# Kernel tuning notes

Measured on AMD Instinct MI355X. Metric: run time of the kernel, lower is better.

The kernel has to match this reference:

```python
import jax, jax.numpy as jnp
import numpy as np

B, CIN, H, W = 4, 2048, 65, 65
NC, INNER, QL = 19, 256, 2975
TEMP = 0.2
EPS = 1e-5


def _conv(x, w, dil=1, pad=0):
    return jax.lax.conv_general_dilated(
        x, w, (1, 1), [(pad, pad), (pad, pad)], rhs_dilation=(dil, dil),
        dimension_numbers=('NCHW', 'OIHW', 'NCHW'))


def _bn_relu(x, g, b):
    # training-mode BatchNorm2d (batch statistics over N,H,W) + ReLU
    m = x.mean(axis=(0, 2, 3), keepdims=True)
    v = x.var(axis=(0, 2, 3), keepdims=True)
    return jax.nn.relu(g[None, :, None, None] * (x - m) * jax.lax.rsqrt(v + EPS)
                       + b[None, :, None, None])


def setup_inputs() -> dict:
    key = jax.random.key(0)
    ks = jax.random.split(key, 12)
    rn = lambda k, s, sc=0.02: jax.random.normal(k, s, jnp.float32) * sc
    inp = {
        'x': jax.random.normal(ks[0], (B, CIN, H, W), jnp.float32),
        # ASPP: global-pool branch (1x1), 1x1 branch, three dilated 3x3 branches
        'w_gp': rn(ks[1], (INNER, CIN, 1, 1)), 'g_gp': jnp.ones(INNER), 'b_gp': jnp.zeros(INNER),
        'w_1x1': rn(ks[2], (INNER, CIN, 1, 1)), 'g_1x1': jnp.ones(INNER), 'b_1x1': jnp.zeros(INNER),
        'w_d12': rn(ks[3], (INNER, CIN, 3, 3)), 'g_d12': jnp.ones(INNER), 'b_d12': jnp.zeros(INNER),
        'w_d24': rn(ks[4], (INNER, CIN, 3, 3)), 'g_d24': jnp.ones(INNER), 'b_d24': jnp.zeros(INNER),
        'w_d36': rn(ks[5], (INNER, CIN, 3, 3)), 'g_d36': jnp.ones(INNER), 'b_d36': jnp.zeros(INNER),
        # head: 3x3 conv on 5*INNER concat -> 256, BN, ReLU (Dropout2d = identity)
        'w_head': rn(ks[6], (256, 5 * INNER, 3, 3)), 'g_head': jnp.ones(256), 'b_head': jnp.zeros(256),
        # final 1x1 classifier
        'w_fin': rn(ks[7], (NC, 256, 1, 1)), 'b_fin': jnp.zeros(NC),
    }
    q = jax.random.normal(ks[8], (NC, INNER, QL), jnp.float32)
    inp['queues'] = q / jnp.linalg.norm(q, axis=1, keepdims=True)  # normalize dim=0 per-class
    return inp


def reference(x, w_gp, g_gp, b_gp, w_1x1, g_1x1, b_1x1,
              w_d12, g_d12, b_d12, w_d24, g_d24, b_d24, w_d36, g_d36, b_d36,
              w_head, g_head, b_head, w_fin, b_fin, queues):
    bsz = x.shape[0]
    # ---- ASPP ----
    gp = x.mean(axis=(2, 3), keepdims=True)                       # global avg pool
    br0 = _bn_relu(_conv(gp, w_gp), g_gp, b_gp)
    br0 = jnp.broadcast_to(br0, (bsz, INNER, x.shape[2], x.shape[3]))
    br1 = _bn_relu(_conv(x, w_1x1), g_1x1, b_1x1)
    br2 = _bn_relu(_conv(x, w_d12, 12, 12), g_d12, b_d12)
    br3 = _bn_relu(_conv(x, w_d24, 24, 24), g_d24, b_d24)
    br4 = _bn_relu(_conv(x, w_d36, 36, 36), g_d36, b_d36)
    aspp_out = jnp.concatenate([br0, br1, br2, br3, br4], axis=1)  # (B, 5*INNER, H, W)
    # ---- head + final (Dropout2d(0.1) treated as identity) ----
    fea = _bn_relu(_conv(aspp_out, w_head, 1, 1), g_head, b_head)  # (B, 256, H, W)
    res = _conv(fea, w_fin) + b_fin[None, :, None, None]           # (B, NC, H, W)
    # ---- construct_region: per-class masked mean over ALL batch pixels ----
    pred = jnp.argmax(res, axis=1).reshape(bsz, -1)                # (B, HW)
    onehot = (pred[:, None, :] == jnp.arange(NC)[None, :, None]).astype(fea.dtype)  # (B,NC,HW)
    feaf = fea.reshape(bsz, 256, -1)                               # (B, 256, HW)
    sums = jnp.einsum('bcp,bkp->kc', feaf, onehot)                 # (NC, 256)
    counts = onehot.sum(axis=(0, 2))                               # (NC,)
    keys = sums / jnp.maximum(counts, 1.0)[:, None]
    keys = keys / jnp.maximum(jnp.linalg.norm(keys, axis=1, keepdims=True), 1e-12)
    present = counts > 0
    # ---- contrast loss: (query . queue)/INNER == mean over channels ----
    sims = jnp.einsum('kc,jcl->kjl', keys, jax.lax.stop_gradient(queues)) / INNER  # (NC,NC,QL)
    a = sims / TEMP
    lse_rows = jax.nn.logsumexp(a, axis=2)                         # (NC, NC)
    neg_rows = jnp.where(jnp.eye(NC, dtype=bool), -jnp.inf, lse_rows)
    lse_neg = jax.nn.logsumexp(neg_rows, axis=1)                   # (NC,) lse over 18*QL negatives
    pos = a[jnp.arange(NC), jnp.arange(NC)]                        # (NC, QL) diagonal class sims
    # CE with label 0 over [pos_i, negs] == logaddexp(pos_i, lse_neg) - pos_i, averaged over QL
    loss_per = (jnp.logaddexp(pos, lse_neg[:, None]) - pos).mean(axis=1)
    contrast_loss = jnp.sum(jnp.where(present, loss_per, 0.0))
    return res, contrast_loss
```

## Files before the change

### kernel.cpp

```cpp
#include <hip/hip_runtime.h>
#include <stdint.h>

#define HW_   4225
#define NPIX_ 16900
#define NC_   19
#define QL_   2975
#define EPSF  1e-5f

#define AS1 __attribute__((address_space(1)))
#define AS3 __attribute__((address_space(3)))

typedef __bf16 bf16x8 __attribute__((ext_vector_type(8)));
typedef float  f32x4  __attribute__((ext_vector_type(4)));

__device__ __forceinline__ unsigned short f2bf(float f) {
    union { float f; unsigned u; } v; v.f = f;
    unsigned u = v.u;
    return (unsigned short)((u + 0x7fffu + ((u >> 16) & 1u)) >> 16);
}
__device__ __forceinline__ float bf2f(unsigned short b) {
    union { unsigned u; float f; } v; v.u = ((unsigned)b) << 16;
    return v.f;
}

__global__ void k_transpose_x(const float* __restrict__ x, unsigned short* __restrict__ xt,
                              float* __restrict__ gp_acc) {
    __shared__ float T[64][66];
    __shared__ float red[256];
    int b  = blockIdx.z;
    int c0 = blockIdx.y * 64;
    int p0 = blockIdx.x * 64;
    int tx = threadIdx.x & 63, ty = threadIdx.x >> 6;
    bool pv = (p0 + tx) < HW_;
    #pragma unroll
    for (int i = 0; i < 16; ++i) {
        int cl = i * 4 + ty;
        T[cl][tx] = pv ? x[((size_t)(b * 2048 + c0 + cl)) * HW_ + p0 + tx] : 0.f;
    }
    __syncthreads();
    #pragma unroll
    for (int i = 0; i < 16; ++i) {
        int pl = i * 4 + ty;
        int p = p0 + pl;
        if (p < HW_) xt[((size_t)(b * HW_ + p)) * 2048 + c0 + tx] = f2bf(T[tx][pl]);
    }
    float s = 0.f;
    #pragma unroll
    for (int k = 0; k < 16; ++k) s += T[tx][ty * 16 + k];
    red[threadIdx.x] = s;
    __syncthreads();
    if (threadIdx.x < 64) {
        float t = red[threadIdx.x] + red[64 + threadIdx.x] + red[128 + threadIdx.x] + red[192 + threadIdx.x];
        atomicAdd(&gp_acc[b * 2048 + c0 + threadIdx.x], t);
    }
}

__global__ void k_wreorder(const float* __restrict__ src, unsigned short* __restrict__ dst,
                           int ci_n, int ntaps) {
    int ci  = blockIdx.x * 256 + threadIdx.x;
    int co  = blockIdx.y, tap = blockIdx.z;
    dst[((size_t)tap * 256 + co) * ci_n + ci] =
        f2bf(src[((size_t)co * ci_n + ci) * ntaps + tap]);
}

__global__ __launch_bounds__(256) void k_conv_gemm(
    const unsigned short* __restrict__ xin, const unsigned short* __restrict__ wr_base,
    unsigned short* __restrict__ out, const unsigned short* __restrict__ zp,
    int cin, int ostride, int is_head)
{
    __shared__ unsigned short As[128 * 64];
    __shared__ unsigned short Bs[128 * 64];
    __shared__ int tapvalid;
    const int tid = threadIdx.x;
    const int bz = blockIdx.z;
    int dil, ntaps, coff;
    if (is_head) { dil = 1; ntaps = 9; coff = 0; }
    else         { dil = 12 * bz; ntaps = bz ? 9 : 1; coff = 256 * (bz + 1); }
    const int mbase = blockIdx.x * 128;
    const int nbase = blockIdx.y * 128;

    const int wv = tid >> 6, lane = tid & 63;
    const int wm = wv >> 1, wn = wv & 1;
    const int quad = lane >> 4, lrow = lane & 15;
    const int sw = lrow & 7;

    const int rowoff = lane >> 3;
    const int lchunk = (lane & 7) ^ rowoff;

    int py4[4], px4[4], pb4[4], pix4[4];
    #pragma unroll
    for (int q = 0; q < 4; ++q) {
        int r = 32 * wv + 8 * q + rowoff;
        int pix = mbase + r;
        pix4[q] = pix;
        int pb = pix / HW_;
        int pr = pix - pb * HW_;
        py4[q] = pr / 65; px4[q] = pr - py4[q] * 65; pb4[q] = pb;
    }

    f32x4 acc[4][4];
    #pragma unroll
    for (int i = 0; i < 4; ++i)
        #pragma unroll
        for (int j = 0; j < 4; ++j) acc[i][j] = (f32x4){0.f, 0.f, 0.f, 0.f};

    for (int tap = 0; tap < ntaps; ++tap) {
        int dy = (ntaps == 1) ? 0 : (tap / 3 - 1) * dil;
        int dx = (ntaps == 1) ? 0 : (tap % 3 - 1) * dil;

        const unsigned short* aptr[4];
        const unsigned short* bptr[4];
        bool av[4];
        bool anyv = false;
        #pragma unroll
        for (int q = 0; q < 4; ++q) {
            int ys = py4[q] + dy, xs = px4[q] + dx;
            bool v = (pix4[q] < NPIX_) && ((unsigned)ys < 65u) && ((unsigned)xs < 65u);
            av[q] = v; anyv |= v;
            aptr[q] = v ? (xin + ((size_t)(pb4[q] * HW_ + ys * 65 + xs)) * cin + lchunk * 8) : zp;
            bptr[q] = wr_base + ((size_t)((bz * 9 + tap) * 256 + nbase + 32 * wv + 8 * q + rowoff)) * cin + lchunk * 8;
        }

        if (tid == 0) tapvalid = 0;
        __syncthreads();
        if (anyv) tapvalid = 1;
        __syncthreads();
        if (!tapvalid) continue;

        for (int kc = 0; kc < cin; kc += 64) {
            __syncthreads();
            #pragma unroll
            for (int q = 0; q < 4; ++q) {
                const unsigned short* pa = av[q] ? (aptr[q] + kc) : zp;
                __builtin_amdgcn_global_load_lds(
                    (const AS1 void*)pa,
                    (AS3 void*)(As + (32 * wv + 8 * q) * 64), 16, 0, 0);
                __builtin_amdgcn_global_load_lds(
                    (const AS1 void*)(bptr[q] + kc),
                    (AS3 void*)(Bs + (32 * wv + 8 * q) * 64), 16, 0, 0);
            }
            __syncthreads();

            #pragma unroll
            for (int kk = 0; kk < 2; ++kk) {
                const int koch = kk * 4 + quad;
                bf16x8 af[4], bfv[4];
                #pragma unroll
                for (int i = 0; i < 4; ++i) {
                    int row = wm * 64 + i * 16 + lrow;
                    af[i] = *(const bf16x8*)(As + row * 64 + ((koch ^ sw) << 3));
                }
                #pragma unroll
                for (int j = 0; j < 4; ++j) {
                    int row = wn * 64 + j * 16 + lrow;
                    bfv[j] = *(const bf16x8*)(Bs + row * 64 + ((koch ^ sw) << 3));
                }
                #pragma unroll
                for (int i = 0; i < 4; ++i)
                    #pragma unroll
                    for (int j = 0; j < 4; ++j)
                        acc[i][j] = __builtin_amdgcn_mfma_f32_16x16x32_bf16(
                            af[i], bfv[j], acc[i][j], 0, 0, 0);
            }
        }
    }

    #pragma unroll
    for (int i = 0; i < 4; ++i) {
        int prow = mbase + wm * 64 + i * 16 + quad * 4;
        #pragma unroll
        for (int r = 0; r < 4; ++r) {
            int p = prow + r;
            if (p < NPIX_) {
                unsigned short* orow = out + (size_t)p * ostride + coff + nbase + wn * 64 + lrow;
                #pragma unroll
                for (int j = 0; j < 4; ++j) orow[j * 16] = f2bf(acc[i][j][r]);
            }
        }
    }
}

__global__ void k_stats(const unsigned short* __restrict__ buf, int stride, int coff,
                        float* __restrict__ sums, float* __restrict__ sumsq) {
    int c = blockIdx.y * 256 + threadIdx.x;
    int p0 = blockIdx.x * 130, p1 = p0 + 130;
    float s = 0.f, q = 0.f;
    for (int p = p0; p < p1; ++p) {
        float v = bf2f(buf[(size_t)p * stride + coff + c]);
        s += v; q += v * v;
    }
    atomicAdd(&sums[c], s);
    atomicAdd(&sumsq[c], q);
}

__global__ void k_br0mv(const float* __restrict__ gp, const float* __restrict__ wgp,
                        float* __restrict__ pre) {
    __shared__ float red[256];
    int co = blockIdx.x, t = threadIdx.x;
    float s0 = 0, s1 = 0, s2 = 0, s3 = 0;
    for (int ci = t; ci < 2048; ci += 256) {
        float w = wgp[(size_t)co * 2048 + ci];
        s0 += w * gp[ci];        s1 += w * gp[2048 + ci];
        s2 += w * gp[4096 + ci]; s3 += w * gp[6144 + ci];
    }
    #pragma unroll
    for (int b = 0; b < 4; ++b) {
        float s = (b == 0) ? s0 : (b == 1) ? s1 : (b == 2) ? s2 : s3;
        red[t] = s; __syncthreads();
        for (int st = 128; st; st >>= 1) { if (t < st) red[t] += red[t + st]; __syncthreads(); }
        if (t == 0) pre[b * 256 + co] = red[0] * (1.0f / HW_);
        __syncthreads();
    }
}

__global__ void k_br0bn(const float* __restrict__ pre, const float* __restrict__ g,
                        const float* __restrict__ bb, float* __restrict__ post) {
    int t = threadIdx.x;
    float v0 = pre[t], v1 = pre[256 + t], v2 = pre[512 + t], v3 = pre[768 + t];
    float m = 0.25f * (v0 + v1 + v2 + v3);
    float var = 0.25f * (v0 * v0 + v1 * v1 + v2 * v2 + v3 * v3) - m * m;
    float sc = g[t] * rsqrtf(var + EPSF), sh = bb[t] - m * sc;
    post[t]       = fmaxf(v0 * sc + sh, 0.f);
    post[256 + t] = fmaxf(v1 * sc + sh, 0.f);
    post[512 + t] = fmaxf(v2 * sc + sh, 0.f);
    post[768 + t] = fmaxf(v3 * sc + sh, 0.f);
}

__global__ void k_norm_aspp(unsigned short* __restrict__ buf,
                            const float* __restrict__ sums, const float* __restrict__ sumsq,
                            const float* __restrict__ g1, const float* __restrict__ b1,
                            const float* __restrict__ g2, const float* __restrict__ b2,
                            const float* __restrict__ g3, const float* __restrict__ b3,
                            const float* __restrict__ g4, const float* __restrict__ b4,
                            const float* __restrict__ br0) {
    int cg = blockIdx.y, t = threadIdx.x;
    int p0 = blockIdx.x * 130, p1 = p0 + 130;
    if (cg == 0) {
        for (int p = p0; p < p1; ++p) {
            int b = p / HW_;
            buf[(size_t)p * 1280 + t] = f2bf(br0[b * 256 + t]);
        }
    } else {
        int c = (cg - 1) * 256 + t;
        float m = sums[c] * (1.f / NPIX_);
        float var = sumsq[c] * (1.f / NPIX_) - m * m;
        const float* g  = (cg == 1) ? g1 : (cg == 2) ? g2 : (cg == 3) ? g3 : g4;
        const float* bb = (cg == 1) ? b1 : (cg == 2) ? b2 : (cg == 3) ? b3 : b4;
        float sc = g[t] * rsqrtf(var + EPSF), sh = bb[t] - m * sc;
        for (int p = p0; p < p1; ++p) {
            size_t idx = (size_t)p * 1280 + cg * 256 + t;
            float v = bf2f(buf[idx]) * sc + sh;
            buf[idx] = f2bf(fmaxf(v, 0.f));
        }
    }
}

__global__ void k_norm_head(unsigned short* __restrict__ buf,
                            const float* __restrict__ sums, const float* __restrict__ sumsq,
                            const float* __restrict__ g, const float* __restrict__ bb) {
    int t = threadIdx.x;
    float m = sums[t] * (1.f / NPIX_);
    float var = sumsq[t] * (1.f / NPIX_) - m * m;
    float sc = g[t] * rsqrtf(var + EPSF), sh = bb[t] - m * sc;
    int p0 = blockIdx.x * 130, p1 = p0 + 130;
    for (int p = p0; p < p1; ++p) {
        size_t idx = (size_t)p * 256 + t;
        float v = bf2f(buf[idx]) * sc + sh;
        buf[idx] = f2bf(fmaxf(v, 0.f));
    }
}

__global__ void k_final(const unsigned short* __restrict__ fea, const float* __restrict__ wfin,
                        const float* __restrict__ bfin, float* __restrict__ outres) {
    int idx = blockIdx.x * 256 + threadIdx.x;
    if (idx >= NPIX_ * NC_) return;
    int p = idx / NC_, k = idx - p * NC_;
    const unsigned short* f = fea + (size_t)p * 256;
    const float* w = wfin + k * 256;
    float acc = 0.f;
    for (int c = 0; c < 256; c += 8) {
        uint4 q = *(const uint4*)(f + c);
        unsigned u0 = q.x, u1 = q.y, u2 = q.z, u3 = q.w;
        acc += bf2f((unsigned short)(u0 & 0xffff)) * w[c + 0];
        acc += bf2f((unsigned short)(u0 >> 16))    * w[c + 1];
        acc += bf2f((unsigned short)(u1 & 0xffff)) * w[c + 2];
        acc += bf2f((unsigned short)(u1 >> 16))    * w[c + 3];
        acc += bf2f((unsigned short)(u2 & 0xffff)) * w[c + 4];
        acc += bf2f((unsigned short)(u2 >> 16))    * w[c + 5];
        acc += bf2f((unsigned short)(u3 & 0xffff)) * w[c + 6];
        acc += bf2f((unsigned short)(u3 >> 16))    * w[c + 7];
    }
    acc += bfin[k];
    int b = p / HW_, yx = p - b * HW_;
    outres[(size_t)(b * NC_ + k) * HW_ + yx] = acc;
}

__global__ void k_argmax(const float* __restrict__ res, int* __restrict__ pred) {
    int p = blockIdx.x * 256 + threadIdx.x;
    if (p >= NPIX_) return;
    int b = p / HW_, yx = p - b * HW_;
    const float* r = res + (size_t)b * NC_ * HW_ + yx;
    float best = r[0]; int bi = 0;
    #pragma unroll
    for (int k = 1; k < NC_; ++k) {
        float v = r[(size_t)k * HW_];
        if (v > best) { best = v; bi = k; }
    }
    pred[p] = bi;
}

__global__ void k_keysums(const unsigned short* __restrict__ fea, const int* __restrict__ pred,
                          float* __restrict__ sums, float* __restrict__ counts) {
    __shared__ float acc[256 * NC_];
    __shared__ float cnt[NC_];
    int t = threadIdx.x;
    #pragma unroll
    for (int k = 0; k < NC_; ++k) acc[t * NC_ + k] = 0.f;
    if (t < NC_) cnt[t] = 0.f;
    __syncthreads();
    int p0 = blockIdx.x * 130, p1 = p0 + 130;
    for (int p = p0; p < p1; ++p) {
        int k = pred[p];
        float v = bf2f(fea[(size_t)p * 256 + t]);
        acc[t * NC_ + k] += v;
        if (t == 0) cnt[k] += 1.f;
    }
    __syncthreads();
    #pragma unroll
    for (int k = 0; k < NC_; ++k) atomicAdd(&sums[k * 256 + t], acc[t * NC_ + k]);
    if (t < NC_) atomicAdd(&counts[t], cnt[t]);
}

__global__ void k_keys(const float* __restrict__ sums, const float* __restrict__ counts,
                       float* __restrict__ keys) {
    __shared__ float red[256];
    int t = threadIdx.x;
    for (int k = 0; k < NC_; ++k) {
        float v = sums[k * 256 + t] / fmaxf(counts[k], 1.f);
        red[t] = v * v; __syncthreads();
        for (int s = 128; s; s >>= 1) { if (t < s) red[t] += red[t + s]; __syncthreads(); }
        float inv = 1.f / fmaxf(sqrtf(red[0]), 1e-12f);
        keys[k * 256 + t] = v * inv;
        __syncthreads();
    }
}

__global__ void k_sims(const float* __restrict__ keys, const float* __restrict__ queues,
                       float* __restrict__ Sexp, float* __restrict__ pos_a) {
    __shared__ float kl[NC_ * 256];
    __shared__ float red[256];
    int t = threadIdx.x;
    int j = blockIdx.x, lc = blockIdx.y;
    #pragma unroll
    for (int k = 0; k < NC_; ++k) kl[k * 256 + t] = keys[k * 256 + t];
    __syncthreads();
    int l = lc * 256 + t;
    bool lv = l < QL_;
    float a[NC_];
    #pragma unroll
    for (int k = 0; k < NC_; ++k) a[k] = 0.f;
    if (lv) {
        const float* q = queues + (size_t)j * 256 * QL_ + l;
        for (int c = 0; c < 256; ++c) {
            float qv = q[(size_t)c * QL_];
            #pragma unroll
            for (int k = 0; k < NC_; ++k) a[k] += kl[k * 256 + c] * qv;
        }
    }
    const float invt = 1.f / (256.f * 0.2f);
    if (lv) pos_a[j * QL_ + l] = a[j] * invt;
    for (int k = 0; k < NC_; ++k) {
        float e = lv ? __expf(a[k] * invt) : 0.f;
        red[t] = e; __syncthreads();
        for (int s = 128; s; s >>= 1) { if (t < s) red[t] += red[t + s]; __syncthreads(); }
        if (t == 0) atomicAdd(&Sexp[k * NC_ + j], red[0]);
        __syncthreads();
    }
}

__global__ void k_loss(const float* __restrict__ Sexp, const float* __restrict__ pos_a,
                       const float* __restrict__ counts, float* __restrict__ out_loss) {
    __shared__ float red[256];
    __shared__ float lseneg[NC_];
    int t = threadIdx.x;
    if (t < NC_) {
        float s = 0.f;
        for (int j = 0; j < NC_; ++j) if (j != t) s += Sexp[t * NC_ + j];
        lseneg[t] = logf(s);
    }
    __syncthreads();
    float total = 0.f;
    for (int k = 0; k < NC_; ++k) {
        float L = lseneg[k];
        float s = 0.f;
        for (int l = t; l < QL_; l += 256) {
            float pos = pos_a[k * QL_ + l];
            float m = fmaxf(pos, L);
            s += logf(__expf(pos - m) + __expf(L - m)) + m - pos;
        }
        red[t] = s; __syncthreads();
        for (int st = 128; st; st >>= 1) { if (t < st) red[t] += red[t + st]; __syncthreads(); }
        if (t == 0 && counts[k] > 0.f) total += red[0] * (1.f / QL_);
        __syncthreads();
    }
    if (t == 0) *out_loss = total;
}

extern "C" void kernel_launch(void* const* d_in, const int* in_sizes, int n_in,
                              void* d_out, int out_size, void* d_ws, size_t ws_size,
                              hipStream_t stream) {
    const float* x      = (const float*)d_in[0];
    const float* w_gp   = (const float*)d_in[1];
    const float* g_gp   = (const float*)d_in[2];
    const float* b_gp   = (const float*)d_in[3];
    const float* w_1x1  = (const float*)d_in[4];
    const float* g_1x1  = (const float*)d_in[5];
    const float* b_1x1  = (const float*)d_in[6];
    const float* w_d12  = (const float*)d_in[7];
    const float* g_d12  = (const float*)d_in[8];
    const float* b_d12  = (const float*)d_in[9];
    const float* w_d24  = (const float*)d_in[10];
    const float* g_d24  = (const float*)d_in[11];
    const float* b_d24  = (const float*)d_in[12];
    const float* w_d36  = (const float*)d_in[13];
    const float* g_d36  = (const float*)d_in[14];
    const float* b_d36  = (const float*)d_in[15];
    const float* w_head = (const float*)d_in[16];
    const float* g_head = (const float*)d_in[17];
    const float* b_head = (const float*)d_in[18];
    const float* w_fin  = (const float*)d_in[19];
    const float* b_fin  = (const float*)d_in[20];
    const float* queues = (const float*)d_in[21];

    char* ws = (char*)d_ws;
    size_t off = 0;
    auto alloc = [&](size_t bytes) { void* p = ws + off; off += (bytes + 255) & ~(size_t)255; return p; };

    unsigned short* x_t     = (unsigned short*)alloc((size_t)4 * HW_ * 2048 * 2);
    unsigned short* wr_aspp = (unsigned short*)alloc((size_t)4 * 9 * 256 * 2048 * 2);
    unsigned short* wr_head = (unsigned short*)alloc((size_t)9 * 256 * 1280 * 2);
    unsigned short* aspp    = (unsigned short*)alloc((size_t)NPIX_ * 1280 * 2);
    unsigned short* headb   = (unsigned short*)alloc((size_t)NPIX_ * 256 * 2);
    float* br0pre  = (float*)alloc(1024 * 4);
    float* br0post = (float*)alloc(1024 * 4);
    int*   pred    = (int*)alloc((size_t)NPIX_ * 4);
    float* pos_a   = (float*)alloc((size_t)NC_ * QL_ * 4);
    float* zbase       = (float*)alloc(16060 * 4);
    unsigned short* zp = (unsigned short*)zbase;
    float* gp          = zbase + 64;
    float* aspp_sums   = zbase + 8256;
    float* aspp_sumsq  = zbase + 9280;
    float* head_sums   = zbase + 10304;
    float* head_sumsq  = zbase + 10560;
    float* key_sums    = zbase + 10816;
    float* counts      = zbase + 15680;
    float* Sexp        = zbase + 15699;
    (void)ws_size; (void)in_sizes; (void)n_in; (void)out_size;

    float* res  = (float*)d_out;
    float* loss = (float*)d_out + (size_t)NPIX_ * NC_;

    hipMemsetAsync(zbase, 0, 16060 * 4, stream);

    k_transpose_x<<<dim3(67, 32, 4), 256, 0, stream>>>(x, x_t, gp);

    k_wreorder<<<dim3(8, 256, 1), 256, 0, stream>>>(w_1x1, wr_aspp, 2048, 1);
    k_wreorder<<<dim3(8, 256, 9), 256, 0, stream>>>(w_d12, wr_aspp + (size_t)1 * 9 * 256 * 2048, 2048, 9);
    k_wreorder<<<dim3(8, 256, 9), 256, 0, stream>>>(w_d24, wr_aspp + (size_t)2 * 9 * 256 * 2048, 2048, 9);
    k_wreorder<<<dim3(8, 256, 9), 256, 0, stream>>>(w_d36, wr_aspp + (size_t)3 * 9 * 256 * 2048, 2048, 9);
    k_wreorder<<<dim3(5, 256, 9), 256, 0, stream>>>(w_head, wr_head, 1280, 9);

    k_conv_gemm<<<dim3(133, 2, 4), 256, 0, stream>>>(x_t, wr_aspp, aspp, zp, 2048, 1280, 0);

    k_stats<<<dim3(130, 4), 256, 0, stream>>>(aspp, 1280, 256, aspp_sums, aspp_sumsq);
    k_br0mv<<<256, 256, 0, stream>>>(gp, w_gp, br0pre);
    k_br0bn<<<1, 256, 0, stream>>>(br0pre, g_gp, b_gp, br0post);
    k_norm_aspp<<<dim3(130, 5), 256, 0, stream>>>(aspp, aspp_sums, aspp_sumsq,
        g_1x1, b_1x1, g_d12, b_d12, g_d24, b_d24, g_d36, b_d36, br0post);

    k_conv_gemm<<<dim3(133, 2, 1), 256, 0, stream>>>(aspp, wr_head, headb, zp, 1280, 256, 1);
    k_stats<<<dim3(130, 1), 256, 0, stream>>>(headb, 256, 0, head_sums, head_sumsq);
    k_norm_head<<<130, 256, 0, stream>>>(headb, head_sums, head_sumsq, g_head, b_head);

    k_final<<<(NPIX_ * NC_ + 255) / 256, 256, 0, stream>>>(headb, w_fin, b_fin, res);
    k_argmax<<<(NPIX_ + 255) / 256, 256, 0, stream>>>(res, pred);
    k_keysums<<<130, 256, 0, stream>>>(headb, pred, key_sums, counts);
    k_keys<<<1, 256, 0, stream>>>(key_sums, counts, (float*)br0pre);
    k_sims<<<dim3(NC_, 12), 256, 0, stream>>>((float*)br0pre, queues, Sexp, pos_a);
    k_loss<<<1, 256, 0, stream>>>(Sexp, pos_a, counts, loss);
}
```

Before: 1.405 ms.

## Widen conv GEMM tile to full 256 outputs and split head taps with atomics

New measurement: 1.539 ms. 1.09x slower.

```diff
diff --git a/kernel.cpp b/kernel.cpp
--- a/kernel.cpp
+++ b/kernel.cpp
@@ -63,27 +63,30 @@
         f2bf(src[((size_t)co * ci_n + ci) * ntaps + tap]);
 }
 
-__global__ __launch_bounds__(256) void k_conv_gemm(
-    const unsigned short* __restrict__ xin, const unsigned short* __restrict__ wr_base,
-    unsigned short* __restrict__ out, const unsigned short* __restrict__ zp,
-    int cin, int ostride, int is_head)
+__global__ __launch_bounds__(256) void k_conv_os(
+    const unsigned short* __restrict__ xin, const unsigned short* __restrict__ wr,
+    unsigned short* __restrict__ outb, float* __restrict__ acc_out,
+    const unsigned short* __restrict__ zp, int cin, int is_head)
 {
     __shared__ unsigned short As[128 * 64];
-    __shared__ unsigned short Bs[128 * 64];
+    __shared__ unsigned short Bs[256 * 64];
     __shared__ int tapvalid;
     const int tid = threadIdx.x;
-    const int bz = blockIdx.z;
-    int dil, ntaps, coff;
-    if (is_head) { dil = 1; ntaps = 9; coff = 0; }
-    else         { dil = 12 * bz; ntaps = bz ? 9 : 1; coff = 256 * (bz + 1); }
+    int dil, tapbeg, tapend, coff, ostride;
+    const unsigned short* wrb;
+    if (is_head) {
+        dil = 1; tapbeg = blockIdx.y * 3; tapend = tapbeg + 3; coff = 0; ostride = 256;
+        wrb = wr;
+    } else {
+        int bz = 3 - blockIdx.y;
+        dil = 12 * bz; tapbeg = 0; tapend = bz ? 9 : 1; coff = 256 * (bz + 1); ostride = 1280;
+        wrb = wr + (size_t)bz * 9 * 256 * cin;
+    }
     const int mbase = blockIdx.x * 128;
-    const int nbase = blockIdx.y * 128;
-
     const int wv = tid >> 6, lane = tid & 63;
     const int wm = wv >> 1, wn = wv & 1;
     const int quad = lane >> 4, lrow = lane & 15;
     const int sw = lrow & 7;
-
     const int rowoff = lane >> 3;
     const int lchunk = (lane & 7) ^ rowoff;
 
@@ -98,18 +101,17 @@
         py4[q] = pr / 65; px4[q] = pr - py4[q] * 65; pb4[q] = pb;
     }
 
-    f32x4 acc[4][4];
+    f32x4 acc[4][8];
     #pragma unroll
     for (int i = 0; i < 4; ++i)
         #pragma unroll
-        for (int j = 0; j < 4; ++j) acc[i][j] = (f32x4){0.f, 0.f, 0.f, 0.f};
-
-    for (int tap = 0; tap < ntaps; ++tap) {
-        int dy = (ntaps == 1) ? 0 : (tap / 3 - 1) * dil;
-        int dx = (ntaps == 1) ? 0 : (tap % 3 - 1) * dil;
+        for (int j = 0; j < 8; ++j) acc[i][j] = (f32x4){0.f, 0.f, 0.f, 0.f};
+
+    for (int tap = tapbeg; tap < tapend; ++tap) {
+        int dy = (tap / 3 - 1) * dil;
+        int dx = (tap % 3 - 1) * dil;
 
         const unsigned short* aptr[4];
-        const unsigned short* bptr[4];
         bool av[4];
         bool anyv = false;
         #pragma unroll
@@ -118,14 +120,14 @@
             bool v = (pix4[q] < NPIX_) && ((unsigned)ys < 65u) && ((unsigned)xs < 65u);
             av[q] = v; anyv |= v;
             aptr[q] = v ? (xin + ((size_t)(pb4[q] * HW_ + ys * 65 + xs)) * cin + lchunk * 8) : zp;
-            bptr[q] = wr_base + ((size_t)((bz * 9 + tap) * 256 + nbase + 32 * wv + 8 * q + rowoff)) * cin + lchunk * 8;
-        }
-
+        }
         if (tid == 0) tapvalid = 0;
         __syncthreads();
         if (anyv) tapvalid = 1;
         __syncthreads();
         if (!tapvalid) continue;
+
+        const unsigned short* bbase = wrb + (size_t)tap * 256 * cin + lchunk * 8;
 
         for (int kc = 0; kc < cin; kc += 64) {
             __syncthreads();
@@ -135,30 +137,33 @@
                 __builtin_amdgcn_global_load_lds(
                     (const AS1 void*)pa,
                     (AS3 void*)(As + (32 * wv + 8 * q) * 64), 16, 0, 0);
+            }
+            #pragma unroll
+            for (int q = 0; q < 8; ++q) {
                 __builtin_amdgcn_global_load_lds(
-                    (const AS1 void*)(bptr[q] + kc),
-                    (AS3 void*)(Bs + (32 * wv + 8 * q) * 64), 16, 0, 0);
+                    (const AS1 void*)(bbase + (size_t)(64 * wv + 8 * q) * cin + kc),
+                    (AS3 void*)(Bs + (64 * wv + 8 * q) * 64), 16, 0, 0);
             }
             __syncthreads();
 
             #pragma unroll
             for (int kk = 0; kk < 2; ++kk) {
                 const int koch = kk * 4 + quad;
-                bf16x8 af[4], bfv[4];
+                bf16x8 af[4], bfv[8];
                 #pragma unroll
                 for (int i = 0; i < 4; ++i) {
                     int row = wm * 64 + i * 16 + lrow;
                     af[i] = *(const bf16x8*)(As + row * 64 + ((koch ^ sw) << 3));
                 }
                 #pragma unroll
-                for (int j = 0; j < 4; ++j) {
-                    int row = wn * 64 + j * 16 + lrow;
+                for (int j = 0; j < 8; ++j) {
+                    int row = wn * 128 + j * 16 + lrow;
                     bfv[j] = *(const bf16x8*)(Bs + row * 64 + ((koch ^ sw) << 3));
                 }
                 #pragma unroll
                 for (int i = 0; i < 4; ++i)
                     #pragma unroll
-                    for (int j = 0; j < 4; ++j)
+                    for (int j = 0; j < 8; ++j)
                         acc[i][j] = __builtin_amdgcn_mfma_f32_16x16x32_bf16(
                             af[i], bfv[j], acc[i][j], 0, 0, 0);
             }
@@ -172,9 +177,15 @@
         for (int r = 0; r < 4; ++r) {
             int p = prow + r;
             if (p < NPIX_) {
-                unsigned short* orow = out + (size_t)p * ostride + coff + nbase + wn * 64 + lrow;
-                #pragma unroll
-                for (int j = 0; j < 4; ++j) orow[j * 16] = f2bf(acc[i][j][r]);
+                if (is_head) {
+                    float* orow = acc_out + (size_t)p * 256 + wn * 128 + lrow;
+                    #pragma unroll
+                    for (int j = 0; j < 8; ++j) atomicAdd(&orow[j * 16], acc[i][j][r]);
+                } else {
+                    unsigned short* orow = outb + (size_t)p * ostride + coff + wn * 128 + lrow;
+                    #pragma unroll
+                    for (int j = 0; j < 8; ++j) orow[j * 16] = f2bf(acc[i][j][r]);
+                }
             }
         }
     }
@@ -187,6 +198,19 @@
     float s = 0.f, q = 0.f;
     for (int p = p0; p < p1; ++p) {
         float v = bf2f(buf[(size_t)p * stride + coff + c]);
+        s += v; q += v * v;
+    }
+    atomicAdd(&sums[c], s);
+    atomicAdd(&sumsq[c], q);
+}
+
+__global__ void k_stats_f32(const float* __restrict__ buf,
+                            float* __restrict__ sums, float* __restrict__ sumsq) {
+    int c = threadIdx.x;
+    int p0 = blockIdx.x * 130, p1 = p0 + 130;
+    float s = 0.f, q = 0.f;
+    for (int p = p0; p < p1; ++p) {
+        float v = buf[(size_t)p * 256 + c];
         s += v; q += v * v;
     }
     atomicAdd(&sums[c], s);
@@ -255,7 +279,7 @@
     }
 }
 
-__global__ void k_norm_head(unsigned short* __restrict__ buf,
+__global__ void k_norm_head(const float* __restrict__ accum, unsigned short* __restrict__ fea,
                             const float* __restrict__ sums, const float* __restrict__ sumsq,
                             const float* __restrict__ g, const float* __restrict__ bb) {
     int t = threadIdx.x;
@@ -265,8 +289,7 @@
     int p0 = blockIdx.x * 130, p1 = p0 + 130;
     for (int p = p0; p < p1; ++p) {
         size_t idx = (size_t)p * 256 + t;
-        float v = bf2f(buf[idx]) * sc + sh;
-        buf[idx] = f2bf(fmaxf(v, 0.f));
+        fea[idx] = f2bf(fmaxf(accum[idx] * sc + sh, 0.f));
     }
 }
 
@@ -455,6 +478,7 @@
     float* key_sums    = zbase + 10816;
     float* counts      = zbase + 15680;
     float* Sexp        = zbase + 15699;
+    float* head_acc = (float*)wr_aspp;
     (void)ws_size; (void)in_sizes; (void)n_in; (void)out_size;
 
     float* res  = (float*)d_out;
@@ -470,7 +494,7 @@
     k_wreorder<<<dim3(8, 256, 9), 256, 0, stream>>>(w_d36, wr_aspp + (size_t)3 * 9 * 256 * 2048, 2048, 9);
     k_wreorder<<<dim3(5, 256, 9), 256, 0, stream>>>(w_head, wr_head, 1280, 9);
 
-    k_conv_gemm<<<dim3(133, 2, 4), 256, 0, stream>>>(x_t, wr_aspp, aspp, zp, 2048, 1280, 0);
+    k_conv_os<<<dim3(133, 4), 256, 0, stream>>>(x_t, wr_aspp, aspp, nullptr, zp, 2048, 0);
 
     k_stats<<<dim3(130, 4), 256, 0, stream>>>(aspp, 1280, 256, aspp_sums, aspp_sumsq);
     k_br0mv<<<256, 256, 0, stream>>>(gp, w_gp, br0pre);
@@ -478,9 +502,10 @@
     k_norm_aspp<<<dim3(130, 5), 256, 0, stream>>>(aspp, aspp_sums, aspp_sumsq,
         g_1x1, b_1x1, g_d12, b_d12, g_d24, b_d24, g_d36, b_d36, br0post);
 
-    k_conv_gemm<<<dim3(133, 2, 1), 256, 0, stream>>>(aspp, wr_head, headb, zp, 1280, 256, 1);
-    k_stats<<<dim3(130, 1), 256, 0, stream>>>(headb, 256, 0, head_sums, head_sumsq);
-    k_norm_head<<<130, 256, 0, stream>>>(headb, head_sums, head_sumsq, g_head, b_head);
+    hipMemsetAsync(head_acc, 0, (size_t)NPIX_ * 256 * 4, stream);
+    k_conv_os<<<dim3(133, 3), 256, 0, stream>>>(aspp, wr_head, nullptr, head_acc, zp, 1280, 1);
+    k_stats_f32<<<130, 256, 0, stream>>>(head_acc, head_sums, head_sumsq);
+    k_norm_head<<<130, 256, 0, stream>>>(head_acc, headb, head_sums, head_sumsq, g_head, b_head);
 
     k_final<<<(NPIX_ * NC_ + 255) / 256, 256, 0, stream>>>(headb, w_fin, b_fin, res);
     k_argmax<<<(NPIX_ + 255) / 256, 256, 0, stream>>>(res, pred);
```

## Split head conv taps across grid z with fp32 partials; fuse final conv and argmax

Applied to the files above, without the earlier changes.

New measurement: 1.429 ms. No clear change (+1.7%).

```diff
diff --git a/kernel.cpp b/kernel.cpp
--- a/kernel.cpp
+++ b/kernel.cpp
@@ -64,18 +64,26 @@
 }
 
 __global__ __launch_bounds__(256) void k_conv_gemm(
-    const unsigned short* __restrict__ xin, const unsigned short* __restrict__ wr_base,
-    unsigned short* __restrict__ out, const unsigned short* __restrict__ zp,
-    int cin, int ostride, int is_head)
+    const unsigned short* __restrict__ xin, const unsigned short* __restrict__ wr,
+    unsigned short* __restrict__ outb, float* __restrict__ outf,
+    const unsigned short* __restrict__ zp, int cin, int ostride, int mode)
 {
     __shared__ unsigned short As[128 * 64];
     __shared__ unsigned short Bs[128 * 64];
     __shared__ int tapvalid;
     const int tid = threadIdx.x;
     const int bz = blockIdx.z;
-    int dil, ntaps, coff;
-    if (is_head) { dil = 1; ntaps = 9; coff = 0; }
-    else         { dil = 12 * bz; ntaps = bz ? 9 : 1; coff = 256 * (bz + 1); }
+    int dil, tapbeg, tapend, coff;
+    const unsigned short* wrb;
+    float* outfg = nullptr;
+    if (mode == 0) {
+        dil = 12 * bz; tapbeg = 0; tapend = bz ? 9 : 1; coff = 256 * (bz + 1);
+        wrb = wr + (size_t)bz * 9 * 256 * cin;
+    } else {
+        dil = 1; tapbeg = 3 * bz; tapend = tapbeg + 3; coff = 0;
+        wrb = wr;
+        outfg = outf + (size_t)bz * NPIX_ * 256;
+    }
     const int mbase = blockIdx.x * 128;
     const int nbase = blockIdx.y * 128;
 
@@ -83,7 +91,6 @@
     const int wm = wv >> 1, wn = wv & 1;
     const int quad = lane >> 4, lrow = lane & 15;
     const int sw = lrow & 7;
-
     const int rowoff = lane >> 3;
     const int lchunk = (lane & 7) ^ rowoff;
 
@@ -104,9 +111,9 @@
         #pragma unroll
         for (int j = 0; j < 4; ++j) acc[i][j] = (f32x4){0.f, 0.f, 0.f, 0.f};
 
-    for (int tap = 0; tap < ntaps; ++tap) {
-        int dy = (ntaps == 1) ? 0 : (tap / 3 - 1) * dil;
-        int dx = (ntaps == 1) ? 0 : (tap % 3 - 1) * dil;
+    for (int tap = tapbeg; tap < tapend; ++tap) {
+        int dy = (tap / 3 - 1) * dil;
+        int dx = (tap % 3 - 1) * dil;
 
         const unsigned short* aptr[4];
         const unsigned short* bptr[4];
@@ -118,7 +125,7 @@
             bool v = (pix4[q] < NPIX_) && ((unsigned)ys < 65u) && ((unsigned)xs < 65u);
             av[q] = v; anyv |= v;
             aptr[q] = v ? (xin + ((size_t)(pb4[q] * HW_ + ys * 65 + xs)) * cin + lchunk * 8) : zp;
-            bptr[q] = wr_base + ((size_t)((bz * 9 + tap) * 256 + nbase + 32 * wv + 8 * q + rowoff)) * cin + lchunk * 8;
+            bptr[q] = wrb + ((size_t)(tap * 256 + nbase + 32 * wv + 8 * q + rowoff)) * cin + lchunk * 8;
         }
 
         if (tid == 0) tapvalid = 0;
@@ -172,9 +179,15 @@
         for (int r = 0; r < 4; ++r) {
             int p = prow + r;
             if (p < NPIX_) {
-                unsigned short* orow = out + (size_t)p * ostride + coff + nbase + wn * 64 + lrow;
-                #pragma unroll
-                for (int j = 0; j < 4; ++j) orow[j * 16] = f2bf(acc[i][j][r]);
+                if (mode == 0) {
+                    unsigned short* orow = outb + (size_t)p * ostride + coff + nbase + wn * 64 + lrow;
+                    #pragma unroll
+                    for (int j = 0; j < 4; ++j) orow[j * 16] = f2bf(acc[i][j][r]);
+                } else {
+                    float* orow = outfg + (size_t)p * 256 + nbase + wn * 64 + lrow;
+                    #pragma unroll
+                    for (int j = 0; j < 4; ++j) orow[j * 16] = acc[i][j][r];
+                }
             }
         }
     }
@@ -187,6 +200,21 @@
     float s = 0.f, q = 0.f;
     for (int p = p0; p < p1; ++p) {
         float v = bf2f(buf[(size_t)p * stride + coff + c]);
+        s += v; q += v * v;
+    }
+    atomicAdd(&sums[c], s);
+    atomicAdd(&sumsq[c], q);
+}
+
+__global__ void k_stats_head(const float* __restrict__ part,
+                             float* __restrict__ sums, float* __restrict__ sumsq) {
+    const size_t NP = (size_t)NPIX_ * 256;
+    int c = threadIdx.x;
+    int p0 = blockIdx.x * 130, p1 = p0 + 130;
+    float s = 0.f, q = 0.f;
+    for (int p = p0; p < p1; ++p) {
+        size_t idx = (size_t)p * 256 + c;
+        float v = part[idx] + part[idx + NP] + part[idx + 2 * NP];
         s += v; q += v * v;
     }
     atomicAdd(&sums[c], s);
@@ -255,9 +283,10 @@
     }
 }
 
-__global__ void k_norm_head(unsigned short* __restrict__ buf,
+__global__ void k_norm_head(const float* __restrict__ part, unsigned short* __restrict__ fea,
                             const float* __restrict__ sums, const float* __restrict__ sumsq,
                             const float* __restrict__ g, const float* __restrict__ bb) {
+    const size_t NP = (size_t)NPIX_ * 256;
     int t = threadIdx.x;
     float m = sums[t] * (1.f / NPIX_);
     float var = sumsq[t] * (1.f / NPIX_) - m * m;
@@ -265,46 +294,40 @@
     int p0 = blockIdx.x * 130, p1 = p0 + 130;
     for (int p = p0; p < p1; ++p) {
         size_t idx = (size_t)p * 256 + t;
-        float v = bf2f(buf[idx]) * sc + sh;
-        buf[idx] = f2bf(fmaxf(v, 0.f));
-    }
-}
-
-__global__ void k_final(const unsigned short* __restrict__ fea, const float* __restrict__ wfin,
-                        const float* __restrict__ bfin, float* __restrict__ outres) {
-    int idx = blockIdx.x * 256 + threadIdx.x;
-    if (idx >= NPIX_ * NC_) return;
-    int p = idx / NC_, k = idx - p * NC_;
+        float v = part[idx] + part[idx + NP] + part[idx + 2 * NP];
+        fea[idx] = f2bf(fmaxf(v * sc + sh, 0.f));
+    }
+}
+
+__global__ __launch_bounds__(256) void k_final_argmax(
+    const unsigned short* __restrict__ fea, const float* __restrict__ wfin,
+    const float* __restrict__ bfin, float* __restrict__ outres, int* __restrict__ pred) {
+    int p = blockIdx.x * 256 + threadIdx.x;
+    if (p >= NPIX_) return;
     const unsigned short* f = fea + (size_t)p * 256;
-    const float* w = wfin + k * 256;
-    float acc = 0.f;
+    float acc[NC_];
+    #pragma unroll
+    for (int k = 0; k < NC_; ++k) acc[k] = bfin[k];
     for (int c = 0; c < 256; c += 8) {
         uint4 q = *(const uint4*)(f + c);
-        unsigned u0 = q.x, u1 = q.y, u2 = q.z, u3 = q.w;
-        acc += bf2f((unsigned short)(u0 & 0xffff)) * w[c + 0];
-        acc += bf2f((unsigned short)(u0 >> 16))    * w[c + 1];
-        acc += bf2f((unsigned short)(u1 & 0xffff)) * w[c + 2];
-        acc += bf2f((unsigned short)(u1 >> 16))    * w[c + 3];
-        acc += bf2f((unsigned short)(u2 & 0xffff)) * w[c + 4];
-        acc += bf2f((unsigned short)(u2 >> 16))    * w[c + 5];
-        acc += bf2f((unsigned short)(u3 & 0xffff)) * w[c + 6];
-        acc += bf2f((unsigned short)(u3 >> 16))    * w[c + 7];
-    }
-    acc += bfin[k];
+        float fv[8];
+        fv[0] = bf2f((unsigned short)(q.x & 0xffff)); fv[1] = bf2f((unsigned short)(q.x >> 16));
+        fv[2] = bf2f((unsigned short)(q.y & 0xffff)); fv[3] = bf2f((unsigned short)(q.y >> 16));
+        fv[4] = bf2f((unsigned short)(q.z & 0xffff)); fv[5] = bf2f((unsigned short)(q.z >> 16));
+        fv[6] = bf2f((unsigned short)(q.w & 0xffff)); fv[7] = bf2f((unsigned short)(q.w >> 16));
+        #pragma unroll
+        for (int k = 0; k < NC_; ++k) {
+            const float* w = wfin + k * 256 + c;
+            #pragma unroll
+            for (int i = 0; i < 8; ++i) acc[k] += fv[i] * w[i];
+        }
+    }
     int b = p / HW_, yx = p - b * HW_;
-    outres[(size_t)(b * NC_ + k) * HW_ + yx] = acc;
-}
-
-__global__ void k_argmax(const float* __restrict__ res, int* __restrict__ pred) {
-    int p = blockIdx.x * 256 + threadIdx.x;
-    if (p >= NPIX_) return;
-    int b = p / HW_, yx = p - b * HW_;
-    const float* r = res + (size_t)b * NC_ * HW_ + yx;
-    float best = r[0]; int bi = 0;
-    #pragma unroll
-    for (int k = 1; k < NC_; ++k) {
-        float v = r[(size_t)k * HW_];
-        if (v > best) { best = v; bi = k; }
+    float best = acc[0]; int bi = 0;
+    #pragma unroll
+    for (int k = 0; k < NC_; ++k) {
+        outres[(size_t)(b * NC_ + k) * HW_ + yx] = acc[k];
+        if (k && acc[k] > best) { best = acc[k]; bi = k; }
     }
     pred[p] = bi;
 }
@@ -455,6 +478,7 @@
     float* key_sums    = zbase + 10816;
     float* counts      = zbase + 15680;
     float* Sexp        = zbase + 15699;
+    float* head_part = (float*)x_t;
     (void)ws_size; (void)in_sizes; (void)n_in; (void)out_size;
 
     float* res  = (float*)d_out;
@@ -470,7 +494,7 @@
     k_wreorder<<<dim3(8, 256, 9), 256, 0, stream>>>(w_d36, wr_aspp + (size_t)3 * 9 * 256 * 2048, 2048, 9);
     k_wreorder<<<dim3(5, 256, 9), 256, 0, stream>>>(w_head, wr_head, 1280, 9);
 
-    k_conv_gemm<<<dim3(133, 2, 4), 256, 0, stream>>>(x_t, wr_aspp, aspp, zp, 2048, 1280, 0);
+    k_conv_gemm<<<dim3(133, 2, 4), 256, 0, stream>>>(x_t, wr_aspp, aspp, nullptr, zp, 2048, 1280, 0);
 
     k_stats<<<dim3(130, 4), 256, 0, stream>>>(aspp, 1280, 256, aspp_sums, aspp_sumsq);
     k_br0mv<<<256, 256, 0, stream>>>(gp, w_gp, br0pre);
@@ -478,12 +502,11 @@
     k_norm_aspp<<<dim3(130, 5), 256, 0, stream>>>(aspp, aspp_sums, aspp_sumsq,
         g_1x1, b_1x1, g_d12, b_d12, g_d24, b_d24, g_d36, b_d36, br0post);
 
-    k_conv_gemm<<<dim3(133, 2, 1), 256, 0, stream>>>(aspp, wr_head, headb, zp, 1280, 256, 1);
-    k_stats<<<dim3(130, 1), 256, 0, stream>>>(headb, 256, 0, head_sums, head_sumsq);
-    k_norm_head<<<130, 256, 0, stream>>>(headb, head_sums, head_sumsq, g_head, b_head);
-
-    k_final<<<(NPIX_ * NC_ + 255) / 256, 256, 0, stream>>>(headb, w_fin, b_fin, res);
-    k_argmax<<<(NPIX_ + 255) / 256, 256, 0, stream>>>(res, pred);
+    k_conv_gemm<<<dim3(133, 2, 3), 256, 0, stream>>>(aspp, wr_head, nullptr, head_part, zp, 1280, 256, 1);
+    k_stats_head<<<130, 256, 0, stream>>>(head_part, head_sums, head_sumsq);
+    k_norm_head<<<130, 256, 0, stream>>>(head_part, headb, head_sums, head_sumsq, g_head, b_head);
+
+    k_final_argmax<<<67, 256, 0, stream>>>(headb, w_fin, b_fin, res, pred);
     k_keysums<<<130, 256, 0, stream>>>(headb, pred, key_sums, counts);
     k_keys<<<1, 256, 0, stream>>>(key_sums, counts, (float*)br0pre);
     k_sims<<<dim3(NC_, 12), 256, 0, stream>>>((float*)br0pre, queues, Sexp, pos_a);
```
